# Kernel tuning notes

Hardware: AMD Instinct MI355X
Metric: run time of the kernel (lower is better)

Reference implementation:

```python
import jax, jax.numpy as jnp
import numpy as np

N_NODES = 50000
N_EDGES = 640000
N_REL = 200
D_IN = 128
D_OUT = 128


def setup_inputs() -> dict:
    key = jax.random.key(0)
    k1, k2, k3, k4, k5, k6 = jax.random.split(key, 6)
    x = jax.random.normal(k1, (N_NODES, D_IN), dtype=jnp.float32)
    edge_index = jax.random.randint(k2, (2, N_EDGES), 0, N_NODES, dtype=jnp.int64)
    edge_type = jax.random.randint(k3, (N_EDGES,), 0, N_REL, dtype=jnp.int64)
    rel_emb = jax.random.normal(k4, (N_REL, D_IN), dtype=jnp.float32)
    # nn.Linear weights stored as [out_features, in_features]
    W_lin = jax.random.normal(k5, (D_OUT, D_IN), dtype=jnp.float32) * (1.0 / np.sqrt(D_IN))
    # xavier_uniform for attn kernel [1, D_IN]
    limit = np.sqrt(6.0 / (1 + D_IN))
    W_attn = jax.random.uniform(k6, (1, D_IN), dtype=jnp.float32, minval=-limit, maxval=limit)
    return {"x": x, "edge_index": edge_index, "edge_type": edge_type,
            "rel_emb": rel_emb, "W_lin": W_lin, "W_attn": W_attn}


def reference(x, edge_index, edge_type, rel_emb, W_lin, W_attn):
    # x: [N, D_in]; edge_index: [2, E]; edge_type: [E]; rel_emb: [R, D_in]
    x_trans = x @ W_lin.T                       # [N, D_out]
    src_idx, tgt_idx = edge_index[0], edge_index[1]
    h_src = x[src_idx]                          # [E, D_in] gather
    h_rel = rel_emb[edge_type]                  # [E, D_in] gather
    sum_feat = h_src + h_rel                    # [E, D_in]
    attn = jax.nn.sigmoid(sum_feat @ W_attn.T)  # [E, 1]
    msg = x_trans[src_idx] * attn               # [E, D_out]
    out = jax.ops.segment_sum(msg, tgt_idx, num_segments=x.shape[0])  # [N, D_out]
    return jax.nn.relu(out)
```

## Files before the change

### kernel.cpp

```cpp
#include <hip/hip_runtime.h>
#include <hip/hip_bf16.h>

#define N_NODES 50000
#define N_EDGES 640000
#define N_REL   200
#define D       128
#define CAP     64

typedef __attribute__((ext_vector_type(8))) short short8;
typedef __attribute__((ext_vector_type(4))) float floatx4;

__device__ __forceinline__ unsigned short f2bf(float f) {
    unsigned u = __float_as_uint(f);
    u += 0x7FFF + ((u >> 16) & 1);
    return (unsigned short)(u >> 16);
}

__device__ __forceinline__ float sigmoidf(float x) {
    return 1.f / (1.f + __expf(-x));
}

__global__ void setup_kernel(const float* __restrict__ W,
                             const float* __restrict__ rel,
                             const float* __restrict__ Wattn,
                             unsigned short* __restrict__ Wbf,
                             float* __restrict__ s_rel,
                             int* __restrict__ count) {
    const int b = blockIdx.x;
    if (b < 64) {
        const int i = b * 256 + threadIdx.x;
        Wbf[i] = f2bf(W[i]);
    } else if (b < 114) {
        const int wave = (b - 64) * 4 + (threadIdx.x >> 6);
        const int lane = threadIdx.x & 63;
        if (wave < N_REL) {
            const float* __restrict__ row = rel + (size_t)wave * D;
            float a = fmaf(row[lane], Wattn[lane],
                           row[lane + 64] * Wattn[lane + 64]);
#pragma unroll
            for (int off = 32; off; off >>= 1)
                a += __shfl_down(a, off);
            if (lane == 0) s_rel[wave] = a;
        }
    } else {
        const int i = (b - 114) * 256 + threadIdx.x;
        if (i < N_NODES) count[i] = 0;
    }
}

__global__ void xtrans_mfma_kernel(const float* __restrict__ x,
                                   const unsigned short* __restrict__ Wbf,
                                   const float* __restrict__ Wattn,
                                   unsigned short* __restrict__ xt,
                                   float* __restrict__ s_node) {
    const int wid = (blockIdx.x * blockDim.x + threadIdx.x) >> 6;
    if (wid >= N_NODES / 16) return;
    const int lane = threadIdx.x & 63;
    const int r16  = lane & 15;
    const int quad = lane >> 4;
    const int m0   = wid * 16;

    short8 af[4];
    float sn = 0.f;
#pragma unroll
    for (int s = 0; s < 4; ++s) {
        const int k0 = s * 32 + quad * 8;
        const float* __restrict__ xr = x + (size_t)(m0 + r16) * D + k0;
        const float4 lo = *(const float4*)(xr);
        const float4 hi = *(const float4*)(xr + 4);
        const float4 wl = *(const float4*)(Wattn + k0);
        const float4 wh = *(const float4*)(Wattn + k0 + 4);
        sn += lo.x * wl.x + lo.y * wl.y + lo.z * wl.z + lo.w * wl.w
            + hi.x * wh.x + hi.y * wh.y + hi.z * wh.z + hi.w * wh.w;
        short8 a;
        a[0] = (short)f2bf(lo.x); a[1] = (short)f2bf(lo.y);
        a[2] = (short)f2bf(lo.z); a[3] = (short)f2bf(lo.w);
        a[4] = (short)f2bf(hi.x); a[5] = (short)f2bf(hi.y);
        a[6] = (short)f2bf(hi.z); a[7] = (short)f2bf(hi.w);
        af[s] = a;
    }
    sn += __shfl_xor(sn, 16);
    sn += __shfl_xor(sn, 32);
    if (quad == 0) s_node[m0 + r16] = sn;

#pragma unroll
    for (int t = 0; t < 8; ++t) {
        floatx4 acc = {0.f, 0.f, 0.f, 0.f};
#pragma unroll
        for (int s = 0; s < 4; ++s) {
            const int k0 = s * 32 + quad * 8;
            const short8 b = *(const short8*)(Wbf + (size_t)(t * 16 + r16) * D + k0);
            acc = __builtin_amdgcn_mfma_f32_16x16x32_bf16(af[s], b, acc, 0, 0, 0);
        }
#pragma unroll
        for (int r = 0; r < 4; ++r) {
            const int orow = m0 + quad * 4 + r;
            xt[(size_t)orow * D + t * 16 + r16] = f2bf(acc[r]);
        }
    }
}

__global__ void bucket_scatter_kernel(const int* __restrict__ src_idx,
                                      const int* __restrict__ tgt_idx,
                                      const int* __restrict__ etype,
                                      const float* __restrict__ s_node,
                                      const float* __restrict__ s_rel,
                                      int* __restrict__ count,
                                      unsigned* __restrict__ sorted) {
    const int e = blockIdx.x * 256 + threadIdx.x;
    if (e >= N_EDGES) return;
    const int s = src_idx[e];
    const int t = tgt_idx[e];
    const int r = etype[e];

    const float logit = s_node[s] + s_rel[r];
    const unsigned rec = ((unsigned)f2bf(sigmoidf(logit)) << 16) | (unsigned)s;

    const int k = atomicAdd(&count[t], 1);
    sorted[t * CAP + k] = rec;
}

__device__ __forceinline__ void gproc(unsigned r, const unsigned short* __restrict__ xt,
                                      int sub, float4& acc) {
    const unsigned src = r & 0xFFFFu;
    const float a = __uint_as_float(r & 0xFFFF0000u);
    const uint2 p = *(const uint2*)(xt + (size_t)src * D + sub * 4);
    acc.x = fmaf(a, __uint_as_float(p.x << 16),        acc.x);
    acc.y = fmaf(a, __uint_as_float(p.x & 0xFFFF0000u), acc.y);
    acc.z = fmaf(a, __uint_as_float(p.y << 16),        acc.z);
    acc.w = fmaf(a, __uint_as_float(p.y & 0xFFFF0000u), acc.w);
}

__global__ void gather_kernel(const int* __restrict__ count,
                              const unsigned* __restrict__ sorted,
                              const unsigned short* __restrict__ xt,
                              float* __restrict__ out) {
    const int wid  = (blockIdx.x * blockDim.x + threadIdx.x) >> 6;
    const int lane = threadIdx.x & 63;
    const int half = lane >> 5;
    const int sub  = lane & 31;
    const int t    = wid * 2 + half;
    if (t >= N_NODES) return;

    const int cnt = count[t];
    const unsigned* __restrict__ rec = sorted + (size_t)t * CAP;

    float4 acc = {0.f, 0.f, 0.f, 0.f};
    int i = 0;
    for (; i + 4 <= cnt; i += 4) {
        const uint4 r4 = *(const uint4*)(rec + i);
        gproc(r4.x, xt, sub, acc);
        gproc(r4.y, xt, sub, acc);
        gproc(r4.z, xt, sub, acc);
        gproc(r4.w, xt, sub, acc);
    }
    for (; i < cnt; ++i)
        gproc(rec[i], xt, sub, acc);

    float4 o;
    o.x = fmaxf(acc.x, 0.f);
    o.y = fmaxf(acc.y, 0.f);
    o.z = fmaxf(acc.z, 0.f);
    o.w = fmaxf(acc.w, 0.f);
    ((float4*)(out + (size_t)t * D))[sub] = o;
}

extern "C" void kernel_launch(void* const* d_in, const int* in_sizes, int n_in,
                              void* d_out, int out_size, void* d_ws, size_t ws_size,
                              hipStream_t stream) {
    const float* x        = (const float*)d_in[0];
    const int*   edge_idx = (const int*)d_in[1];
    const int*   etype    = (const int*)d_in[2];
    const float* rel_emb  = (const float*)d_in[3];
    const float* W_lin    = (const float*)d_in[4];
    const float* W_attn   = (const float*)d_in[5];
    float* out = (float*)d_out;

    const int* src_idx = edge_idx;
    const int* tgt_idx = edge_idx + N_EDGES;

    unsigned short* xt   = (unsigned short*)d_ws;
    float* s_node        = (float*)(xt + (size_t)N_NODES * D);
    float* s_rel         = s_node + N_NODES;
    unsigned short* Wbf  = (unsigned short*)(s_rel + N_REL);
    int*   count         = (int*)(Wbf + D * D);
    unsigned* sorted     = (unsigned*)(count + N_NODES);

    setup_kernel<<<dim3(310), dim3(256), 0, stream>>>(
        W_lin, rel_emb, W_attn, Wbf, s_rel, count);

    {
        const int waves = N_NODES / 16;
        const int blocks = (waves * 64 + 255) / 256;
        xtrans_mfma_kernel<<<dim3(blocks), dim3(256), 0, stream>>>(
            x, Wbf, W_attn, xt, s_node);
    }

    bucket_scatter_kernel<<<dim3((N_EDGES + 255) / 256), dim3(256), 0, stream>>>(
        src_idx, tgt_idx, etype, s_node, s_rel, count, sorted);

    gather_kernel<<<dim3(N_NODES / 8), dim3(256), 0, stream>>>(
        count, sorted, xt, out);
}
```

Before: 170.4 us.

## Move node attention scores to setup and fuse GEMM with edge bucketing

Node attention logits s_node move from the MFMA transform kernel into the setup kernel as extra blocks. The transform GEMM and the edge bucket-scatter then share one launch, interleaving one GEMM block per three scatter blocks. This removes a kernel launch boundary and lets the compute-bound GEMM overlap the atomic- and memory-bound scatter. The cost is that x is read twice (once for the scores, once for the GEMM) and the setup kernel becomes larger.

Result: slower. 176.0 us (+3.3%).

```diff
diff --git a/kernel.cpp b/kernel.cpp
--- a/kernel.cpp
+++ b/kernel.cpp
@@ -21,10 +21,12 @@
 }
 
 __global__ void setup_kernel(const float* __restrict__ W,
+                             const float* __restrict__ x,
                              const float* __restrict__ rel,
                              const float* __restrict__ Wattn,
                              unsigned short* __restrict__ Wbf,
                              float* __restrict__ s_rel,
+                             float* __restrict__ s_node,
                              int* __restrict__ count) {
     const int b = blockIdx.x;
     if (b < 64) {
@@ -42,82 +44,87 @@
                 a += __shfl_down(a, off);
             if (lane == 0) s_rel[wave] = a;
         }
-    } else {
+    } else if (b < 310) {
         const int i = (b - 114) * 256 + threadIdx.x;
         if (i < N_NODES) count[i] = 0;
+    } else {
+        const int node = (b - 310) * 8 + (threadIdx.x >> 5);
+        const int sub  = threadIdx.x & 31;
+        if (node < N_NODES) {
+            const float4 xv = ((const float4*)(x + (size_t)node * D))[sub];
+            const float4 wv = ((const float4*)Wattn)[sub];
+            float a = xv.x * wv.x + xv.y * wv.y + xv.z * wv.z + xv.w * wv.w;
+#pragma unroll
+            for (int off = 16; off; off >>= 1)
+                a += __shfl_xor(a, off);
+            if (sub == 0) s_node[node] = a;
+        }
     }
 }
 
-__global__ void xtrans_mfma_kernel(const float* __restrict__ x,
-                                   const unsigned short* __restrict__ Wbf,
-                                   const float* __restrict__ Wattn,
-                                   unsigned short* __restrict__ xt,
-                                   float* __restrict__ s_node) {
-    const int wid = (blockIdx.x * blockDim.x + threadIdx.x) >> 6;
-    if (wid >= N_NODES / 16) return;
-    const int lane = threadIdx.x & 63;
-    const int r16  = lane & 15;
-    const int quad = lane >> 4;
-    const int m0   = wid * 16;
-
-    short8 af[4];
-    float sn = 0.f;
-#pragma unroll
-    for (int s = 0; s < 4; ++s) {
-        const int k0 = s * 32 + quad * 8;
-        const float* __restrict__ xr = x + (size_t)(m0 + r16) * D + k0;
-        const float4 lo = *(const float4*)(xr);
-        const float4 hi = *(const float4*)(xr + 4);
-        const float4 wl = *(const float4*)(Wattn + k0);
-        const float4 wh = *(const float4*)(Wattn + k0 + 4);
-        sn += lo.x * wl.x + lo.y * wl.y + lo.z * wl.z + lo.w * wl.w
-            + hi.x * wh.x + hi.y * wh.y + hi.z * wh.z + hi.w * wh.w;
-        short8 a;
-        a[0] = (short)f2bf(lo.x); a[1] = (short)f2bf(lo.y);
-        a[2] = (short)f2bf(lo.z); a[3] = (short)f2bf(lo.w);
-        a[4] = (short)f2bf(hi.x); a[5] = (short)f2bf(hi.y);
-        a[6] = (short)f2bf(hi.z); a[7] = (short)f2bf(hi.w);
-        af[s] = a;
-    }
-    sn += __shfl_xor(sn, 16);
-    sn += __shfl_xor(sn, 32);
-    if (quad == 0) s_node[m0 + r16] = sn;
-
-#pragma unroll
-    for (int t = 0; t < 8; ++t) {
-        floatx4 acc = {0.f, 0.f, 0.f, 0.f};
+__global__ void fused_kernel(const float* __restrict__ x,
+                             const unsigned short* __restrict__ Wbf,
+                             unsigned short* __restrict__ xt,
+                             const int* __restrict__ src_idx,
+                             const int* __restrict__ tgt_idx,
+                             const int* __restrict__ etype,
+                             const float* __restrict__ s_node,
+                             const float* __restrict__ s_rel,
+                             int* __restrict__ count,
+                             unsigned* __restrict__ sorted) {
+    const int b = blockIdx.x;
+    if ((b & 3) == 3) {
+        const int wid = (b >> 2) * 4 + (threadIdx.x >> 6);
+        if (wid >= N_NODES / 16) return;
+        const int lane = threadIdx.x & 63;
+        const int r16  = lane & 15;
+        const int quad = lane >> 4;
+        const int m0   = wid * 16;
+
+        short8 af[4];
 #pragma unroll
         for (int s = 0; s < 4; ++s) {
             const int k0 = s * 32 + quad * 8;
-            const short8 b = *(const short8*)(Wbf + (size_t)(t * 16 + r16) * D + k0);
-            acc = __builtin_amdgcn_mfma_f32_16x16x32_bf16(af[s], b, acc, 0, 0, 0);
-        }
-#pragma unroll
-        for (int r = 0; r < 4; ++r) {
-            const int orow = m0 + quad * 4 + r;
-            xt[(size_t)orow * D + t * 16 + r16] = f2bf(acc[r]);
-        }
+            const float* __restrict__ xr = x + (size_t)(m0 + r16) * D + k0;
+            const float4 lo = *(const float4*)(xr);
+            const float4 hi = *(const float4*)(xr + 4);
+            short8 a;
+            a[0] = (short)f2bf(lo.x); a[1] = (short)f2bf(lo.y);
+            a[2] = (short)f2bf(lo.z); a[3] = (short)f2bf(lo.w);
+            a[4] = (short)f2bf(hi.x); a[5] = (short)f2bf(hi.y);
+            a[6] = (short)f2bf(hi.z); a[7] = (short)f2bf(hi.w);
+            af[s] = a;
+        }
+
+#pragma unroll
+        for (int t = 0; t < 8; ++t) {
+            floatx4 acc = {0.f, 0.f, 0.f, 0.f};
+#pragma unroll
+            for (int s = 0; s < 4; ++s) {
+                const int k0 = s * 32 + quad * 8;
+                const short8 bb = *(const short8*)(Wbf + (size_t)(t * 16 + r16) * D + k0);
+                acc = __builtin_amdgcn_mfma_f32_16x16x32_bf16(af[s], bb, acc, 0, 0, 0);
+            }
+#pragma unroll
+            for (int r = 0; r < 4; ++r) {
+                const int orow = m0 + quad * 4 + r;
+                xt[(size_t)orow * D + t * 16 + r16] = f2bf(acc[r]);
+            }
+        }
+    } else {
+        const int sb = b - (b >> 2);
+        const int e = sb * 256 + threadIdx.x;
+        if (e >= N_EDGES) return;
+        const int s = src_idx[e];
+        const int t = tgt_idx[e];
+        const int r = etype[e];
+
+        const float logit = s_node[s] + s_rel[r];
+        const unsigned rec = ((unsigned)f2bf(sigmoidf(logit)) << 16) | (unsigned)s;
+
+        const int k = atomicAdd(&count[t], 1);
+        sorted[t * CAP + k] = rec;
     }
-}
-
-__global__ void bucket_scatter_kernel(const int* __restrict__ src_idx,
-                                      const int* __restrict__ tgt_idx,
-                                      const int* __restrict__ etype,
-                                      const float* __restrict__ s_node,
-                                      const float* __restrict__ s_rel,
-                                      int* __restrict__ count,
-                                      unsigned* __restrict__ sorted) {
-    const int e = blockIdx.x * 256 + threadIdx.x;
-    if (e >= N_EDGES) return;
-    const int s = src_idx[e];
-    const int t = tgt_idx[e];
-    const int r = etype[e];
-
-    const float logit = s_node[s] + s_rel[r];
-    const unsigned rec = ((unsigned)f2bf(sigmoidf(logit)) << 16) | (unsigned)s;
-
-    const int k = atomicAdd(&count[t], 1);
-    sorted[t * CAP + k] = rec;
 }
 
 __device__ __forceinline__ void gproc(unsigned r, const unsigned short* __restrict__ xt,
@@ -186,18 +193,11 @@
     int*   count         = (int*)(Wbf + D * D);
     unsigned* sorted     = (unsigned*)(count + N_NODES);
 
-    setup_kernel<<<dim3(310), dim3(256), 0, stream>>>(
-        W_lin, rel_emb, W_attn, Wbf, s_rel, count);
-
-    {
-        const int waves = N_NODES / 16;
-        const int blocks = (waves * 64 + 255) / 256;
-        xtrans_mfma_kernel<<<dim3(blocks), dim3(256), 0, stream>>>(
-            x, Wbf, W_attn, xt, s_node);
-    }
-
-    bucket_scatter_kernel<<<dim3((N_EDGES + 255) / 256), dim3(256), 0, stream>>>(
-        src_idx, tgt_idx, etype, s_node, s_rel, count, sorted);
+    setup_kernel<<<dim3(310 + (N_NODES + 7) / 8), dim3(256), 0, stream>>>(
+        W_lin, x, rel_emb, W_attn, Wbf, s_rel, s_node, count);
+
+    fused_kernel<<<dim3(3333), dim3(256), 0, stream>>>(
+        x, Wbf, xt, src_idx, tgt_idx, etype, s_node, s_rel, count, sorted);
 
     gather_kernel<<<dim3(N_NODES / 8), dim3(256), 0, stream>>>(
         count, sorted, xt, out);
```
